# Performance work log

Hardware: AMD Instinct MI355X
Metric: run time of the kernel (lower is better)

Reference implementation:

```python
import jax, jax.numpy as jnp
import numpy as np

K_TOP = 16
TEMP = 1.0
EPS = 1e-9

def setup_inputs() -> dict:
    key = jax.random.key(0)
    k1, k2, k3 = jax.random.split(key, 3)
    B, H, N, D = 4, 8, 2048, 64
    q = jax.random.normal(k1, (B, H, N, D), dtype=jnp.float32)
    k = jax.random.normal(k2, (B, H, N, D), dtype=jnp.float32)
    u = jax.random.uniform(k3, (B, N, N), dtype=jnp.float32)
    return {"q": q, "k": k, "u": u}

def reference(q, k, u):
    # q, k: [B, H, N, D]; u: uniform noise [B, N, N]
    d_head = q.shape[-1]
    scale = 1.0 / jnp.sqrt(jnp.asarray(d_head, dtype=q.dtype))
    # [B, H, N, N] scores, then mean over heads -> [B, N, N]
    attn_scores = jnp.einsum('bhnd,bhmd->bhnm', q, k) * scale
    logits = attn_scores.mean(axis=1)
    gumbel = -jnp.log(-jnp.log(u + EPS) + EPS)
    probs = jax.nn.softmax((logits + gumbel) / TEMP, axis=-1)
    topk_vals = jax.lax.top_k(probs, K_TOP)[0]          # [B, N, K]
    thresh = topk_vals.min(axis=-1, keepdims=True)      # [B, N, 1]
    sparse_mask = (probs >= thresh).astype(probs.dtype)
    return sparse_mask[:, None, :, :]                   # [B, 1, N, N]
```

## Files before the change

### kernel.cpp

```cpp
#include <hip/hip_runtime.h>
#include <math.h>

#define BB 4
#define HH 8
#define NN 2048
#define DD 64
#define KTOP 16
#define CUT_MARGIN 1e-3f

typedef _Float16 half_t;
typedef __attribute__((ext_vector_type(8))) _Float16 half8;
typedef __attribute__((ext_vector_type(4))) float floatx4;

__device__ __forceinline__ void gl_lds16f(const float* g, float* l) {
    __builtin_amdgcn_global_load_lds(
        (const __attribute__((address_space(1))) void*)g,
        (__attribute__((address_space(3))) void*)l, 16, 0, 0);
}

__global__ __launch_bounds__(256, 2) void gemm_f32stage(const float* __restrict__ q,
                                                        const float* __restrict__ kk,
                                                        float* __restrict__ L) {
    const int b  = blockIdx.z;
    const int i0 = blockIdx.y * 128;
    const int j0 = blockIdx.x * 128;
    const int tid  = threadIdx.x;
    const int wave = __builtin_amdgcn_readfirstlane(tid >> 6);
    const int lane = tid & 63;
    const int wr = wave >> 1, wc = wave & 1;
    const int lm = lane & 15, quad = lane >> 4;

    __shared__ __align__(16) float Asm[8192];
    __shared__ __align__(16) float Bsm[8192];

    const int w2 = wave & 1;
    const float* gbase;
    float* lbase;
    if (wave < 2) { gbase = q  + ((size_t)(b * HH) * NN + i0) * DD; lbase = Asm; }
    else          { gbase = kk + ((size_t)(b * HH) * NN + j0) * DD; lbase = Bsm; }

    floatx4 acc1[4][4], acc2[4][4];
#pragma unroll
    for (int tr = 0; tr < 4; ++tr)
#pragma unroll
        for (int tc = 0; tc < 4; ++tc) {
            acc1[tr][tc] = (floatx4)0.0f;
            acc2[tr][tc] = (floatx4)0.0f;
        }

    for (int hh = 0; hh < HH; ++hh) {
        const float* gs = gbase + (size_t)hh * (NN * DD);
        __syncthreads();
#pragma unroll
        for (int i = 0; i < 16; ++i) {
            const int P   = (w2 << 10) + (i << 6) + lane;
            const int lin = (P & ~7) | ((P & 7) ^ ((i & 1) << 2) ^ quad);
            gl_lds16f(gs + (size_t)lin * 4,
                      lbase + (size_t)((w2 << 10) + (i << 6)) * 4);
        }
        __syncthreads();

#pragma unroll
        for (int ks = 0; ks < 2; ++ks) {
            half8 ah[4], al[4], bh[4], bl[4];
#pragma unroll
            for (int t = 0; t < 4; ++t) {
                {
                    const int am = wr * 64 + t * 16 + lm;
                    const int u0 = am * 16 + ks * 8 + quad * 2;
                    const int p0 = (u0 & ~7) | ((u0 & 7) ^ (am & 7));
                    float4 f0 = *(const float4*)&Asm[p0 * 4];
                    float4 f1 = *(const float4*)&Asm[(p0 ^ 1) * 4];
                    float a[8] = {f0.x, f0.y, f0.z, f0.w, f1.x, f1.y, f1.z, f1.w};
#pragma unroll
                    for (int e = 0; e < 8; ++e) {
                        half_t hq = (half_t)a[e];
                        ah[t][e] = hq;
                        al[t][e] = (half_t)((a[e] - (float)hq) * 2048.0f);
                    }
                }
                {
                    const int bm = wc * 64 + t * 16 + lm;
                    const int u0 = bm * 16 + ks * 8 + quad * 2;
                    const int p0 = (u0 & ~7) | ((u0 & 7) ^ (bm & 7));
                    float4 f0 = *(const float4*)&Bsm[p0 * 4];
                    float4 f1 = *(const float4*)&Bsm[(p0 ^ 1) * 4];
                    float a[8] = {f0.x, f0.y, f0.z, f0.w, f1.x, f1.y, f1.z, f1.w};
#pragma unroll
                    for (int e = 0; e < 8; ++e) {
                        half_t hq = (half_t)a[e];
                        bh[t][e] = hq;
                        bl[t][e] = (half_t)((a[e] - (float)hq) * 2048.0f);
                    }
                }
            }
            __builtin_amdgcn_s_setprio(1);
#pragma unroll
            for (int tr = 0; tr < 4; ++tr)
#pragma unroll
                for (int tc = 0; tc < 4; ++tc) {
                    acc1[tr][tc] = __builtin_amdgcn_mfma_f32_16x16x32_f16(
                        ah[tr], bh[tc], acc1[tr][tc], 0, 0, 0);
                    acc2[tr][tc] = __builtin_amdgcn_mfma_f32_16x16x32_f16(
                        ah[tr], bl[tc], acc2[tr][tc], 0, 0, 0);
                    acc2[tr][tc] = __builtin_amdgcn_mfma_f32_16x16x32_f16(
                        al[tr], bh[tc], acc2[tr][tc], 0, 0, 0);
                }
            __builtin_amdgcn_s_setprio(0);
        }
    }

    const float s1 = 0.015625f;
    const float s2 = 0.015625f / 2048.0f;
#pragma unroll
    for (int tr = 0; tr < 4; ++tr)
#pragma unroll
        for (int r = 0; r < 4; ++r) {
            const int grow = i0 + wr * 64 + tr * 16 + quad * 4 + r;
            float* Lp = L + ((size_t)b * NN + grow) * NN + j0 + wc * 64 + lm;
#pragma unroll
            for (int tc = 0; tc < 4; ++tc)
                Lp[tc * 16] = acc1[tr][tc][r] * s1 + acc2[tr][tc][r] * s2;
        }
}

__device__ __forceinline__ unsigned long long flip64(double x) {
    unsigned long long v = (unsigned long long)__double_as_longlong(x);
    return v ^ ((0ULL - (v >> 63)) | 0x8000000000000000ULL);
}
__device__ __forceinline__ double unflip64(unsigned long long k) {
    unsigned long long v = (k >> 63) ? (k ^ 0x8000000000000000ULL) : ~k;
    return __longlong_as_double((long long)v);
}

__global__ __launch_bounds__(256) void topk_mask(float* __restrict__ LM,
                                                 const float* __restrict__ u) {
    const int wave = threadIdx.x >> 6;
    const int lane = threadIdx.x & 63;
    const int row  = blockIdx.x * 4 + wave;
    float* lrow = LM + (size_t)row * NN;
    const float* urow = u + (size_t)row * NN;

    __shared__ int s_idx[4][64];

    float z[32];
    unsigned hard = 0;
    float4 lb = *(const float4*)(lrow + lane * 4);
    float4 ub = *(const float4*)(urow + lane * 4);
#pragma unroll
    for (int e = 0; e < 8; ++e) {
        float4 lnx, unx;
        if (e < 7) {
            lnx = *(const float4*)(lrow + (e + 1) * 256 + lane * 4);
            unx = *(const float4*)(urow + (e + 1) * 256 + lane * 4);
        }
        const float* ls = (const float*)&lb;
        const float* us = (const float*)&ub;
#pragma unroll
        for (int s = 0; s < 4; ++s) {
            float w = -__logf(us[s] + 1e-9f);
            z[e * 4 + s] = ls[s] - __logf(w + 1e-9f);
            hard |= (us[s] > 0.999f ? 1u : 0u) << (e * 4 + s);
        }
        lb = lnx; ub = unx;
    }

    float v = z[0];
#pragma unroll
    for (int r = 1; r < 32; ++r) v = fmaxf(v, z[r]);
#pragma unroll
    for (int kS = 2; kS <= 64; kS <<= 1) {
#pragma unroll
        for (int j = kS >> 1; j > 0; j >>= 1) {
            float o = __shfl_xor(v, j, 64);
            bool asc = ((lane & kS) == 0);
            bool lower = ((lane & j) == 0);
            float mn = fminf(v, o), mx = fmaxf(v, o);
            v = (asc == lower) ? mn : mx;
        }
    }
    const float cut = __shfl(v, 48, 64) - CUT_MARGIN;

    int c = 0;
#pragma unroll
    for (int r = 0; r < 32; ++r) {
        bool p = (z[r] >= cut);
        unsigned long long m = __ballot(p);
        if (p) {
            int slot = c + __popcll(m & ((1ULL << lane) - 1ULL));
            if (slot < 64) s_idx[wave][slot] = (r >> 2) * 256 + lane * 4 + (r & 3);
        }
        c += __popcll(m);
    }
    if (c > 64) c = 64;

    unsigned long long key = 0xFFFFFFFFFFFFFFFFULL;
    if (lane < c) {
        int idx = s_idx[wave][lane];
        double uu = (double)urow[idx] + 1e-9;
        double w  = -log(uu);
        double g  = -log(w + 1e-9);
        key = flip64((double)lrow[idx] + g);
    }
#pragma unroll
    for (int kS = 2; kS <= 64; kS <<= 1) {
#pragma unroll
        for (int j = kS >> 1; j > 0; j >>= 1) {
            unsigned long long o = __shfl_xor(key, j, 64);
            bool asc = ((lane & kS) == 0);
            bool lower = ((lane & j) == 0);
            unsigned long long mn = (key < o) ? key : o;
            unsigned long long mx = (key < o) ? o : key;
            key = (asc == lower) ? mn : mx;
        }
    }
    const double thresh = unflip64(__shfl(key, c - KTOP, 64));

    const float t_hi = (float)thresh + 3e-4f;
    const float t_lo = (float)thresh - 3e-4f;
    unsigned bm = hard;
#pragma unroll
    for (int r = 0; r < 32; ++r)
        bm |= ((z[r] <= t_hi && z[r] >= t_lo) ? 1u : 0u) << r;
    while (bm) {
        int t = __builtin_ctz(bm);
        bm &= bm - 1;
        const int idx = (t >> 2) * 256 + lane * 4 + (t & 3);
        double uu = (double)urow[idx] + 1e-9;
        double w  = -log(uu);
        double g  = -log(w + 1e-9);
        double z64 = (double)lrow[idx] + g;
        z[t] = (z64 >= thresh) ? 1.0e30f : -1.0e30f;
    }

#pragma unroll
    for (int e = 0; e < 8; ++e) {
        float o[4];
#pragma unroll
        for (int s = 0; s < 4; ++s)
            o[s] = (z[e * 4 + s] > t_hi) ? 1.0f : 0.0f;
        *(float4*)(lrow + e * 256 + lane * 4) = *(float4*)o;
    }
}

extern "C" void kernel_launch(void* const* d_in, const int* in_sizes, int n_in,
                              void* d_out, int out_size, void* d_ws, size_t ws_size,
                              hipStream_t stream) {
    const float* q = (const float*)d_in[0];
    const float* k = (const float*)d_in[1];
    const float* u = (const float*)d_in[2];
    float* out = (float*)d_out;
    (void)d_ws; (void)ws_size;

    dim3 grid1(NN / 128, NN / 128, BB);
    gemm_f32stage<<<grid1, 256, 0, stream>>>(q, k, out);

    topk_mask<<<BB * NN / 4, 256, 0, stream>>>(out, u);
}
```

Baseline: 224.0 us.

## Convert f32 tiles to split fp16 once at LDS staging and swizzle block order

Tiles are now loaded from global into registers and converted to fp16 hi/lo pairs before being stored in LDS, instead of staging raw fp32 via global_load_lds and converting inside the MFMA loop. Each element is converted once per block rather than once per wave that reads it, and MFMA operands come straight from LDS as half8 loads. The grid is flattened with a block-index swizzle so neighbouring blocks share q/k tiles in cache. In exchange the asynchronous direct-to-LDS load is lost, register pressure goes up from the staged float4 values, and the new LDS layout may cause bank conflicts.

```diff
diff --git a/kernel.cpp b/kernel.cpp
--- a/kernel.cpp
+++ b/kernel.cpp
@@ -12,32 +12,28 @@
 typedef __attribute__((ext_vector_type(8))) _Float16 half8;
 typedef __attribute__((ext_vector_type(4))) float floatx4;
 
-__device__ __forceinline__ void gl_lds16f(const float* g, float* l) {
-    __builtin_amdgcn_global_load_lds(
-        (const __attribute__((address_space(1))) void*)g,
-        (__attribute__((address_space(3))) void*)l, 16, 0, 0);
-}
-
-__global__ __launch_bounds__(256, 2) void gemm_f32stage(const float* __restrict__ q,
-                                                        const float* __restrict__ kk,
-                                                        float* __restrict__ L) {
-    const int b  = blockIdx.z;
-    const int i0 = blockIdx.y * 128;
-    const int j0 = blockIdx.x * 128;
+__global__ __launch_bounds__(256, 2) void gemm_conv(const float* __restrict__ q,
+                                                    const float* __restrict__ kk,
+                                                    float* __restrict__ L) {
+    const int flat = blockIdx.x;
+    const int swz  = (flat & 7) * 128 + (flat >> 3);
+    const int j0 = (swz & 15) * 128;
+    const int i0 = ((swz >> 4) & 15) * 128;
+    const int b  = swz >> 8;
+
     const int tid  = threadIdx.x;
     const int wave = __builtin_amdgcn_readfirstlane(tid >> 6);
     const int lane = tid & 63;
     const int wr = wave >> 1, wc = wave & 1;
     const int lm = lane & 15, quad = lane >> 4;
 
-    __shared__ __align__(16) float Asm[8192];
-    __shared__ __align__(16) float Bsm[8192];
-
-    const int w2 = wave & 1;
-    const float* gbase;
-    float* lbase;
-    if (wave < 2) { gbase = q  + ((size_t)(b * HH) * NN + i0) * DD; lbase = Asm; }
-    else          { gbase = kk + ((size_t)(b * HH) * NN + j0) * DD; lbase = Bsm; }
+    __shared__ __align__(16) half_t Ah[8192];
+    __shared__ __align__(16) half_t Al[8192];
+    __shared__ __align__(16) half_t Bh[8192];
+    __shared__ __align__(16) half_t Bl[8192];
+
+    const float* gA = q  + ((size_t)(b * HH) * NN + i0) * DD;
+    const float* gB = kk + ((size_t)(b * HH) * NN + j0) * DD;
 
     floatx4 acc1[4][4], acc2[4][4];
 #pragma unroll
@@ -49,50 +45,57 @@
         }
 
     for (int hh = 0; hh < HH; ++hh) {
-        const float* gs = gbase + (size_t)hh * (NN * DD);
+        const float* ga = gA + (size_t)hh * (NN * DD);
+        const float* gb = gB + (size_t)hh * (NN * DD);
+
         __syncthreads();
-#pragma unroll
-        for (int i = 0; i < 16; ++i) {
-            const int P   = (w2 << 10) + (i << 6) + lane;
-            const int lin = (P & ~7) | ((P & 7) ^ ((i & 1) << 2) ^ quad);
-            gl_lds16f(gs + (size_t)lin * 4,
-                      lbase + (size_t)((w2 << 10) + (i << 6)) * 4);
-        }
+
+        float4 v0[8], v1[8];
+#pragma unroll
+        for (int i = 0; i < 4; ++i) {
+            const int p = i * 256 + tid;
+            v0[i]     = *(const float4*)(ga + (size_t)p * 8);
+            v1[i]     = *(const float4*)(ga + (size_t)p * 8 + 4);
+            v0[4 + i] = *(const float4*)(gb + (size_t)p * 8);
+            v1[4 + i] = *(const float4*)(gb + (size_t)p * 8 + 4);
+        }
+#pragma unroll
+        for (int i = 0; i < 8; ++i) {
+            const int p  = (i & 3) * 256 + tid;
+            const int r  = p >> 3;
+            const int u8 = p & 7;
+            const int off = (u8 >> 2) * 4096 + (r >> 3) * 256 +
+                            (u8 & 3) * 64 + (r & 7) * 8;
+            half_t* dh = (i < 4) ? Ah : Bh;
+            half_t* dl = (i < 4) ? Al : Bl;
+            float a[8] = {v0[i].x, v0[i].y, v0[i].z, v0[i].w,
+                          v1[i].x, v1[i].y, v1[i].z, v1[i].w};
+            half8 h, l;
+#pragma unroll
+            for (int e = 0; e < 8; ++e) {
+                half_t hv = (half_t)a[e];
+                h[e] = hv;
+                l[e] = (half_t)((a[e] - (float)hv) * 2048.0f);
+            }
+            *(half8*)&dh[off] = h;
+            *(half8*)&dl[off] = l;
+        }
+
         __syncthreads();
 
 #pragma unroll
         for (int ks = 0; ks < 2; ++ks) {
-            half8 ah[4], al[4], bh[4], bl[4];
+            half8 fah[4], fal[4], fbh[4], fbl[4];
 #pragma unroll
             for (int t = 0; t < 4; ++t) {
-                {
-                    const int am = wr * 64 + t * 16 + lm;
-                    const int u0 = am * 16 + ks * 8 + quad * 2;
-                    const int p0 = (u0 & ~7) | ((u0 & 7) ^ (am & 7));
-                    float4 f0 = *(const float4*)&Asm[p0 * 4];
-                    float4 f1 = *(const float4*)&Asm[(p0 ^ 1) * 4];
-                    float a[8] = {f0.x, f0.y, f0.z, f0.w, f1.x, f1.y, f1.z, f1.w};
-#pragma unroll
-                    for (int e = 0; e < 8; ++e) {
-                        half_t hq = (half_t)a[e];
-                        ah[t][e] = hq;
-                        al[t][e] = (half_t)((a[e] - (float)hq) * 2048.0f);
-                    }
-                }
-                {
-                    const int bm = wc * 64 + t * 16 + lm;
-                    const int u0 = bm * 16 + ks * 8 + quad * 2;
-                    const int p0 = (u0 & ~7) | ((u0 & 7) ^ (bm & 7));
-                    float4 f0 = *(const float4*)&Bsm[p0 * 4];
-                    float4 f1 = *(const float4*)&Bsm[(p0 ^ 1) * 4];
-                    float a[8] = {f0.x, f0.y, f0.z, f0.w, f1.x, f1.y, f1.z, f1.w};
-#pragma unroll
-                    for (int e = 0; e < 8; ++e) {
-                        half_t hq = (half_t)a[e];
-                        bh[t][e] = hq;
-                        bl[t][e] = (half_t)((a[e] - (float)hq) * 2048.0f);
-                    }
-                }
+                const int am = wr * 64 + t * 16 + lm;
+                const int bm = wc * 64 + t * 16 + lm;
+                const int ai = ks * 4096 + ((am >> 3) << 8) + (quad << 6) + ((am & 7) << 3);
+                const int bi = ks * 4096 + ((bm >> 3) << 8) + (quad << 6) + ((bm & 7) << 3);
+                fah[t] = *(const half8*)&Ah[ai];
+                fal[t] = *(const half8*)&Al[ai];
+                fbh[t] = *(const half8*)&Bh[bi];
+                fbl[t] = *(const half8*)&Bl[bi];
             }
             __builtin_amdgcn_s_setprio(1);
 #pragma unroll
@@ -100,11 +103,11 @@
 #pragma unroll
                 for (int tc = 0; tc < 4; ++tc) {
                     acc1[tr][tc] = __builtin_amdgcn_mfma_f32_16x16x32_f16(
-                        ah[tr], bh[tc], acc1[tr][tc], 0, 0, 0);
+                        fah[tr], fbh[tc], acc1[tr][tc], 0, 0, 0);
                     acc2[tr][tc] = __builtin_amdgcn_mfma_f32_16x16x32_f16(
-                        ah[tr], bl[tc], acc2[tr][tc], 0, 0, 0);
+                        fah[tr], fbl[tc], acc2[tr][tc], 0, 0, 0);
                     acc2[tr][tc] = __builtin_amdgcn_mfma_f32_16x16x32_f16(
-                        al[tr], bh[tc], acc2[tr][tc], 0, 0, 0);
+                        fal[tr], fbh[tc], acc2[tr][tc], 0, 0, 0);
                 }
             __builtin_amdgcn_s_setprio(0);
         }
@@ -252,8 +255,7 @@
     float* out = (float*)d_out;
     (void)d_ws; (void)ws_size;
 
-    dim3 grid1(NN / 128, NN / 128, BB);
-    gemm_f32stage<<<grid1, 256, 0, stream>>>(q, k, out);
+    gemm_conv<<<(NN / 128) * (NN / 128) * BB, 256, 0, stream>>>(q, k, out);
 
     topk_mask<<<BB * NN / 4, 256, 0, stream>>>(out, u);
 }
```

New measurement: 244.4 us. +9.1%, slower.
